# Optimization experiments

Measured on AMD Instinct MI355X. Metric: run time of the kernel, lower is better.

Reference implementation:

```python
import jax, jax.numpy as jnp
import numpy as np

NEG_SLOPE = 0.01
LN_EPS = 1e-5


def leaky_relu(x):
    return jax.nn.leaky_relu(x, NEG_SLOPE)


def layer_norm(x, w, b):
    mu = jnp.mean(x, axis=-1, keepdims=True)
    var = jnp.var(x, axis=-1, keepdims=True)
    return (x - mu) * jax.lax.rsqrt(var + LN_EPS) * w + b


def setup_inputs() -> dict:
    key = jax.random.key(0)
    B, N, IN_DIM, OUT_DIM = 16, 1024, 512, 512
    ks = jax.random.split(key, 12)
    s_in = 1.0 / np.sqrt(IN_DIM)
    s_n = 1.0 / np.sqrt(N)
    return {
        "node_feats": jax.random.normal(ks[0], (B, N, IN_DIM), jnp.float32),
        "adj_matrix": jax.random.uniform(ks[1], (B, N, N), jnp.float32),
        "linear_w": jax.random.uniform(ks[2], (OUT_DIM, IN_DIM), jnp.float32, -s_in, s_in),
        "linear_b": jax.random.uniform(ks[3], (OUT_DIM,), jnp.float32, -s_in, s_in),
        "q_w": jax.random.uniform(ks[4], (N, N), jnp.float32, -s_n, s_n),
        "q_b": jax.random.uniform(ks[5], (N,), jnp.float32, -s_n, s_n),
        "k_w": jax.random.uniform(ks[6], (N, N), jnp.float32, -s_n, s_n),
        "k_b": jax.random.uniform(ks[7], (N,), jnp.float32, -s_n, s_n),
        "v_w": jax.random.uniform(ks[8], (N, N), jnp.float32, -s_n, s_n),
        "v_b": jax.random.uniform(ks[9], (N,), jnp.float32, -s_n, s_n),
        "norm1_w": jnp.ones((N,), jnp.float32),
        "norm1_b": jnp.zeros((N,), jnp.float32),
        "norm2_w": jnp.ones((OUT_DIM,), jnp.float32),
        "norm2_b": jnp.zeros((OUT_DIM,), jnp.float32),
        "edge_weight": jnp.ones((N, N), jnp.float32),
    }


def reference(node_feats, adj_matrix, linear_w, linear_b, q_w, q_b, k_w, k_b,
              v_w, v_b, norm1_w, norm1_b, norm2_w, norm2_b, edge_weight):
    N = edge_weight.shape[0]
    channel_scale = N ** (-0.5)

    # weighted adjacency + symmetric degree normalization (D^-1/2 A D^-1/2)
    W_A = adj_matrix * jax.nn.sigmoid(edge_weight)          # [B,N,N]
    d_inv_sqrt = jnp.power(jnp.sum(W_A, axis=-1), -0.5)     # [B,N]
    d_inv_sqrt = jnp.where(jnp.isinf(d_inv_sqrt), 0.0, d_inv_sqrt)
    W_A = d_inv_sqrt[:, :, None] * W_A * d_inv_sqrt[:, None, :]

    # node projection + channel-wise self-attention
    X = leaky_relu(jnp.einsum('bni,oi->bno', node_feats, linear_w) + linear_b)  # [B,N,O]
    Tx = jnp.swapaxes(X, -1, -2)                             # [B,O,N]
    Tx = layer_norm(Tx, norm1_w, norm1_b)
    q = jnp.einsum('bxh,gh->bxg', Tx, q_w) + q_b
    k = jnp.einsum('bxh,gh->bxg', Tx, k_w) + k_b
    v = leaky_relu(jnp.einsum('bxh,gh->bxg', Tx, v_w) + v_b)
    att = jax.nn.softmax(jnp.einsum('bxh,byh->bxy', q, k) * channel_scale, axis=-1)
    Tx = Tx + jnp.einsum('bxy,byh->bxh', att, v)

    # graph propagation + final norm
    X = jnp.swapaxes(Tx, -1, -2)                             # [B,N,O]
    X = jnp.einsum('bnm,bmo->bno', W_A, X)
    return layer_norm(X, norm2_w, norm2_b)
```

## Files before the change

kernel.cpp:

```cpp
#include <hip/hip_runtime.h>


typedef __bf16 bf16x8 __attribute__((ext_vector_type(8)));
typedef float  f32x4  __attribute__((ext_vector_type(4)));

#define DEV __device__ __forceinline__

DEV float bf2f(unsigned short u) {
  union { unsigned i; float f; } x; x.i = ((unsigned)u) << 16; return x.f;
}
DEV unsigned short f2bf(float f) {
  unsigned u = __float_as_uint(f);
  u += 0x7fffu + ((u >> 16) & 1u);
  return (unsigned short)(u >> 16);
}
DEV float sigmoidf_(float x) { return 1.0f / (1.0f + __expf(-x)); }

DEV float wave_sum(float v) {
#pragma unroll
  for (int o = 32; o > 0; o >>= 1) v += __shfl_xor(v, o, 64);
  return v;
}
DEV float wave_max(float v) {
#pragma unroll
  for (int o = 32; o > 0; o >>= 1) v = fmaxf(v, __shfl_xor(v, o, 64));
  return v;
}

DEV void gload16(const unsigned short* g, unsigned short* l) {
  __builtin_amdgcn_global_load_lds(
      (const __attribute__((address_space(1))) unsigned int*)g,
      (__attribute__((address_space(3))) unsigned int*)l, 16, 0, 0);
}

#define BAR()        asm volatile("s_barrier" ::: "memory")
#define WAIT_VM(n)   asm volatile("s_waitcnt vmcnt(" #n ")" ::: "memory")
#define SB0()        __builtin_amdgcn_sched_barrier(0)

__global__ __launch_bounds__(256) void cast_kernel(const float* __restrict__ in,
                                                   unsigned short* __restrict__ out,
                                                   int n4) {
  int g = blockIdx.x * 256 + threadIdx.x;
  if (g >= n4) return;
  float4 v = *(const float4*)(in + (size_t)g * 4);
  ushort4 o;
  o.x = f2bf(v.x); o.y = f2bf(v.y); o.z = f2bf(v.z); o.w = f2bf(v.w);
  *(ushort4*)(out + (size_t)g * 4) = o;
}

__global__ __launch_bounds__(256) void sigrow_kernel(const float* __restrict__ adj,
                                                     const float* __restrict__ edge,
                                                     float* __restrict__ dis) {
  __shared__ float sh[4];
  size_t row = blockIdx.x;
  int n = (int)(row & 1023);
  const float* ar = adj + row * 1024;
  const float* er = edge + (size_t)n * 1024;
  int c = threadIdx.x * 4;
  float4 a4 = *(const float4*)(ar + c);
  float4 e4 = *(const float4*)(er + c);
  float s = a4.x * sigmoidf_(e4.x) + a4.y * sigmoidf_(e4.y) +
            a4.z * sigmoidf_(e4.z) + a4.w * sigmoidf_(e4.w);
  s = wave_sum(s);
  if ((threadIdx.x & 63) == 0) sh[threadIdx.x >> 6] = s;
  __syncthreads();
  if (threadIdx.x == 0) {
    float t = sh[0] + sh[1] + sh[2] + sh[3];
    dis[row] = t > 0.0f ? rsqrtf(t) : 0.0f;
  }
}

__global__ __launch_bounds__(256) void wa_kernel(const float* __restrict__ adj,
                                                 const float* __restrict__ edge,
                                                 const float* __restrict__ dis,
                                                 unsigned short* __restrict__ wa) {
  size_t g = (size_t)blockIdx.x * 256 + threadIdx.x;
  int m = (int)(g & 255) * 4;
  size_t rest = g >> 8;
  int n = (int)(rest & 1023);
  int b = (int)(rest >> 10);
  float4 a4 = *(const float4*)(adj + rest * 1024 + m);
  float4 e4 = *(const float4*)(edge + (size_t)n * 1024 + m);
  float dn = dis[rest];
  float4 dm = *(const float4*)(dis + (size_t)b * 1024 + m);
  ushort4 o;
  o.x = f2bf(dn * a4.x * sigmoidf_(e4.x) * dm.x);
  o.y = f2bf(dn * a4.y * sigmoidf_(e4.y) * dm.y);
  o.z = f2bf(dn * a4.z * sigmoidf_(e4.z) * dm.z);
  o.w = f2bf(dn * a4.w * sigmoidf_(e4.w) * dm.w);
  *(ushort4*)(wa + g * 4) = o;
}

template <int VPT, bool OUTF32>
__global__ __launch_bounds__(256) void ln_kernel(const unsigned short* __restrict__ in,
                                                 const float* __restrict__ gw,
                                                 const float* __restrict__ gb,
                                                 void* __restrict__ out, int D) {
  __shared__ float sh[8];
  size_t row = blockIdx.x;
  const unsigned short* x = in + row * (size_t)D;
  int base = threadIdx.x * VPT;
  float v[VPT];
  if (VPT == 4) {
    ushort4 u = *(const ushort4*)(x + base);
    v[0] = bf2f(u.x); v[1] = bf2f(u.y); v[2] = bf2f(u.z); v[3] = bf2f(u.w);
  } else {
    ushort2 u = *(const ushort2*)(x + base);
    v[0] = bf2f(u.x); v[1] = bf2f(u.y);
  }
  float s = 0.f, sq = 0.f;
#pragma unroll
  for (int i = 0; i < VPT; i++) { s += v[i]; sq += v[i] * v[i]; }
  s = wave_sum(s); sq = wave_sum(sq);
  if ((threadIdx.x & 63) == 0) { sh[threadIdx.x >> 6] = s; sh[4 + (threadIdx.x >> 6)] = sq; }
  __syncthreads();
  s = sh[0] + sh[1] + sh[2] + sh[3];
  sq = sh[4] + sh[5] + sh[6] + sh[7];
  float mean = s / D;
  float var = sq / D - mean * mean;
  float rs = rsqrtf(fmaxf(var, 0.0f) + 1e-5f);
#pragma unroll
  for (int i = 0; i < VPT; i++) {
    float y = (v[i] - mean) * rs * gw[base + i] + gb[base + i];
    if (OUTF32) ((float*)out)[row * D + base + i] = y;
    else        ((unsigned short*)out)[row * D + base + i] = f2bf(y);
  }
}

__global__ __launch_bounds__(256) void softmax_kernel(const float* __restrict__ in,
                                                      const float* __restrict__ in2,
                                                      unsigned short* __restrict__ out) {
  __shared__ float sh[4];
  size_t row = blockIdx.x;
  const float* x = in + row * 512;
  const float* x2 = in2 + row * 512;
  float2 u = *(const float2*)(x + threadIdx.x * 2);
  float2 u2 = *(const float2*)(x2 + threadIdx.x * 2);
  float a = (u.x + u2.x) * 0.03125f, b = (u.y + u2.y) * 0.03125f;
  float m = wave_max(fmaxf(a, b));
  int wid = threadIdx.x >> 6;
  if ((threadIdx.x & 63) == 0) sh[wid] = m;
  __syncthreads();
  m = fmaxf(fmaxf(sh[0], sh[1]), fmaxf(sh[2], sh[3]));
  __syncthreads();
  float e0 = __expf(a - m), e1 = __expf(b - m);
  float s = wave_sum(e0 + e1);
  if ((threadIdx.x & 63) == 0) sh[wid] = s;
  __syncthreads();
  s = sh[0] + sh[1] + sh[2] + sh[3];
  float inv = 1.0f / s;
  ushort2 o; o.x = f2bf(e0 * inv); o.y = f2bf(e1 * inv);
  *(ushort2*)(out + row * 512 + threadIdx.x * 2) = o;
}

#define MFMA16(d, s0, s1) d = __builtin_amdgcn_mfma_f32_16x16x32_bf16(s0, s1, d, 0, 0, 0)

#define STGA(bi, h, kt) do { \
  gload16(gA + (size_t)((h) * 128) * Kr + (size_t)(kt) * 64, As + (bi) * 16384 + (h) * 8192 + ldst); \
  gload16(gA + (size_t)((h) * 128 + 64) * Kr + (size_t)(kt) * 64, As + (bi) * 16384 + (h) * 8192 + 4096 + ldst); \
} while (0)
#define STGB(bi, h, kt) do { \
  gload16(gB + (size_t)((h) * 128) * Kr + (size_t)(kt) * 64, Bs + (bi) * BSZ + (h) * 8192 + ldst); \
  gload16(gB + (size_t)((h) * 128 + 64) * Kr + (size_t)(kt) * 64, Bs + (bi) * BSZ + (h) * 8192 + 4096 + ldst); \
} while (0)

#define LDA(bi, mh) do { \
  _Pragma("unroll") for (int mf = 0; mf < 4; mf++) { \
    a[mf][0] = *(const bf16x8*)&As[(bi) * 16384 + arow + ((mh) * 4 + mf) * 1024 + xs0]; \
    a[mf][1] = *(const bf16x8*)&As[(bi) * 16384 + arow + ((mh) * 4 + mf) * 1024 + xs1]; \
  } } while (0)
#define LDB(bi, nh) do { \
  if constexpr (BNT == 256) { \
    _Pragma("unroll") for (int nf = 0; nf < 2; nf++) { \
      bb[(nh) * 2 + nf][0] = *(const bf16x8*)&Bs[(bi) * BSZ + brow + ((nh) * 2 + nf) * 1024 + xs0]; \
      bb[(nh) * 2 + nf][1] = *(const bf16x8*)&Bs[(bi) * BSZ + brow + ((nh) * 2 + nf) * 1024 + xs1]; \
    } \
  } else { \
    _Pragma("unroll") for (int nf = 0; nf < 2; nf++) { \
      bb[nf][0] = *(const bf16x8*)&Bs[(bi) * BSZ + brow + nf * 1024 + xs0]; \
      bb[nf][1] = *(const bf16x8*)&Bs[(bi) * BSZ + brow + nf * 1024 + xs1]; \
    } \
  } } while (0)

#define MMQB(mh, nh) do { \
  if constexpr (BNT == 256) { \
    _Pragma("unroll") for (int mf = 0; mf < 4; mf++) \
    _Pragma("unroll") for (int nf = 0; nf < 2; nf++) { \
      MFMA16(acc[(mh) * 4 + mf][(nh) * 2 + nf], a[mf][0], bb[(nh) * 2 + nf][0]); \
      MFMA16(acc[(mh) * 4 + mf][(nh) * 2 + nf], a[mf][1], bb[(nh) * 2 + nf][1]); \
    } \
  } else { \
    _Pragma("unroll") for (int mf = 0; mf < 4; mf++) { \
      MFMA16(acc[(mh) * 4 + mf][(nh)], a[mf][0], bb[(nh)][0]); \
      MFMA16(acc[(mh) * 4 + mf][(nh)], a[mf][1], bb[(nh)][1]); \
    } \
  } } while (0)

#define MMQ2(mh) do { \
  __builtin_amdgcn_s_setprio(1); \
  MMQB(mh, 0); MMQB(mh, 1); \
  __builtin_amdgcn_s_setprio(0); } while (0)

#define TILE2(P, kt, SA, SB, EW) do { \
  EW; BAR(); \
  LDA(P, 0); LDB(P, 0); \
  if constexpr (BNT == 256) { LDB(P, 1); } \
  if (SA) { STGA((P) ^ 1, 0, (kt) + 1); STGA((P) ^ 1, 1, (kt) + 1); } \
  BAR(); SB0(); MMQ2(0); SB0(); BAR(); \
  LDA(P, 1); \
  if (SB) { STGB(P, 0, (kt) + 2); if constexpr (BNT == 256) { STGB(P, 1, (kt) + 2); } } \
  BAR(); SB0(); MMQ2(1); SB0(); \
} while (0)

template <int BNT, int BIAS , bool LEAKY, bool RESID,
          bool OUTF32, bool SPLIT, bool SPLITK>
__global__ __launch_bounds__(512, 2) void gemm256(
    const unsigned short* __restrict__ A, size_t sA,
    const unsigned short* __restrict__ Bt, size_t sB,
    const float* __restrict__ bias, const float* __restrict__ bias2,
    const unsigned short* __restrict__ resid,
    void* __restrict__ out, void* __restrict__ out2,
    int M, int NcS, int K, int Kst, int lgx, int lgy, int xh) {
  constexpr int NFR = (BNT == 256) ? 4 : 2;
  constexpr int BSZ = BNT * 64;
  __shared__ unsigned short As[2 * 16384];
  __shared__ unsigned short Bs[2 * BSZ];
  const int qc = gridDim.x >> 3;
  const int dd = blockIdx.x;
  const int lb = (dd & 7) * qc + (dd >> 3);
  const int x = lb & ((1 << lgx) - 1);
  const int y = (lb >> lgx) & ((1 << lgy) - 1);
  const int b = (lb >> (lgx + lgy)) & 15;
  const int sk = SPLITK ? (lb >> (lgx + lgy + 4)) : 0;

  const int tid = threadIdx.x;
  const int wid = tid >> 6, lane = tid & 63;
  const int wr = wid >> 2, wc = wid & 3;
  const int l15 = lane & 15, l4 = lane >> 4;
  const int tM = y * 256, tN = x * BNT;
  const size_t Kr = (size_t)Kst;

  const int srow = wid * 8 + (lane >> 3);
  const int scol = ((lane & 7) ^ ((lane >> 3) & 7)) * 8;
  const int koff = sk * K;
  const unsigned short* gA = A + sA * b + (size_t)(tM + srow) * Kr + scol + koff;
  const unsigned short* gB = Bt + sB * b + (size_t)(tN + srow) * Kr + scol + koff;
  const int ldst = wid * 512;

  const int xs0 = ((0 * 4 + l4) ^ (lane & 7)) * 8;
  const int xs1 = ((1 * 4 + l4) ^ (lane & 7)) * 8;
  const int arow = (wr * 128 + l15) * 64;
  const int brow = (wc * (BNT / 4) + l15) * 64;

  f32x4 acc[8][NFR] = {};
  bf16x8 a[4][2], bb[NFR][2];

  const int nt = K >> 6;
  STGB(0, 0, 0);
  if constexpr (BNT == 256) { STGB(0, 1, 0); }
  STGA(0, 0, 0); STGA(0, 1, 0);
  STGB(1, 0, 1);
  if constexpr (BNT == 256) { STGB(1, 1, 1); }

  if constexpr (BNT == 256) {
    for (int kt = 0; kt < nt - 2; kt += 2) {
      TILE2(0, kt, true, true, WAIT_VM(4));
      TILE2(1, kt + 1, true, true, WAIT_VM(4));
    }
    TILE2(0, nt - 2, true, false, WAIT_VM(4));
    TILE2(1, nt - 1, false, false, WAIT_VM(0));
  } else {
    for (int kt = 0; kt < nt - 2; kt += 2) {
      TILE2(0, kt, true, true, WAIT_VM(2));
      TILE2(1, kt + 1, true, true, WAIT_VM(2));
    }
    TILE2(0, nt - 2, true, false, WAIT_VM(2));
    TILE2(1, nt - 1, false, false, WAIT_VM(0));
  }

  const float* bia = bias;
  void* o = out;
  if (SPLIT && x >= xh) { bia = bias2; o = out2; }
  if (SPLITK && sk) o = out2;
  const size_t ob = (size_t)M * NcS * b;
#pragma unroll
  for (int mf = 0; mf < 8; mf++)
#pragma unroll
    for (int nf = 0; nf < NFR; nf++) {
      const int cg = tN + wc * (BNT / 4) + nf * 16 + l15;
      const int rbase = tM + wr * 128 + mf * 16 + l4 * 4;
#pragma unroll
      for (int r = 0; r < 4; r++) {
        const int rg = rbase + r;
        float v = acc[mf][nf][r];
        if (BIAS == 1) v += bia[rg];
        if (BIAS == 2) v += bia[cg];
        if (LEAKY) v = v > 0.0f ? v : 0.01f * v;
        const size_t idx = ob + (size_t)rg * NcS + cg;
        if (RESID) v += bf2f(resid[idx]);
        if (OUTF32) ((float*)o)[idx] = v;
        else        ((unsigned short*)o)[idx] = f2bf(v);
      }
    }
}

extern "C" void kernel_launch(void* const* d_in, const int* in_sizes, int n_in,
                              void* d_out, int out_size, void* d_ws, size_t ws_size,
                              hipStream_t stream) {
  const float* node_feats = (const float*)d_in[0];
  const float* adj        = (const float*)d_in[1];
  const float* linear_w   = (const float*)d_in[2];
  const float* linear_b   = (const float*)d_in[3];
  const float* q_w        = (const float*)d_in[4];
  const float* q_b        = (const float*)d_in[5];
  const float* k_w        = (const float*)d_in[6];
  const float* k_b        = (const float*)d_in[7];
  const float* v_w        = (const float*)d_in[8];
  const float* v_b        = (const float*)d_in[9];
  const float* n1w        = (const float*)d_in[10];
  const float* n1b        = (const float*)d_in[11];
  const float* n2w        = (const float*)d_in[12];
  const float* n2b        = (const float*)d_in[13];
  const float* edge       = (const float*)d_in[14];
  float* out = (float*)d_out;

  const int B = 16, N = 1024, C = 512;
  const size_t MiB = 1u << 20;
  char* w = (char*)d_ws;
  unsigned short* nf_bf   = (unsigned short*)(w);
  unsigned short* Xt_bf   = (unsigned short*)(w + 16 * MiB);
  float*          att_raw = (float*)(w);
  float*          att_raw2= (float*)(w + 16 * MiB);
  unsigned short* WA_bf   = (unsigned short*)(w);
  unsigned short* Txln    = (unsigned short*)(w + 32 * MiB);
  unsigned short* q_bf    = (unsigned short*)(w + 48 * MiB);
  unsigned short* X3_bf   = (unsigned short*)(w + 48 * MiB);
  unsigned short* k_bf    = (unsigned short*)(w + 64 * MiB);
  unsigned short* att_bf  = (unsigned short*)(w + 64 * MiB);
  unsigned short* vt_bf   = (unsigned short*)(w + 80 * MiB);
  unsigned short* Tx2_bf  = (unsigned short*)(w + 96 * MiB);
  unsigned short* lw_bf   = (unsigned short*)(w + 112 * MiB);
  unsigned short* qw_bf   = (unsigned short*)(w + 113 * MiB);
  unsigned short* kw_bf   = (unsigned short*)(w + 115 * MiB);
  unsigned short* vw_bf   = (unsigned short*)(w + 117 * MiB);
  float*          dis     = (float*)(w + 119 * MiB);

  cast_kernel<<<(B * N * C / 4 + 255) / 256, 256, 0, stream>>>(node_feats, nf_bf, B * N * C / 4);
  cast_kernel<<<(C * C / 4 + 255) / 256, 256, 0, stream>>>(linear_w, lw_bf, C * C / 4);
  cast_kernel<<<(N * N / 4 + 255) / 256, 256, 0, stream>>>(q_w, qw_bf, N * N / 4);
  cast_kernel<<<(N * N / 4 + 255) / 256, 256, 0, stream>>>(k_w, kw_bf, N * N / 4);
  cast_kernel<<<(N * N / 4 + 255) / 256, 256, 0, stream>>>(v_w, vw_bf, N * N / 4);

  sigrow_kernel<<<B * N, 256, 0, stream>>>(adj, edge, dis);

  gemm256<128, 1, true, false, false, false, false><<<256, 512, 0, stream>>>(
      lw_bf, 0, nf_bf, (size_t)N * C, linear_b, nullptr, nullptr,
      Xt_bf, nullptr, C, N, C, C, 3, 1, 999);

  ln_kernel<4, false><<<B * C, 256, 0, stream>>>(Xt_bf, n1w, n1b, Txln, N);

  gemm256<256, 2, false, false, false, true, false><<<256, 512, 0, stream>>>(
      Txln, (size_t)C * N, qw_bf, 0, q_b, k_b - 1024, nullptr,
      q_bf, (void*)(k_bf - 1024), C, N, N, N, 3, 1, 4);

  gemm256<128, 1, true, false, false, false, false><<<256, 512, 0, stream>>>(
      vw_bf, 0, Txln, (size_t)C * N, v_b, nullptr, nullptr,
      vt_bf, nullptr, N, C, N, N, 2, 2, 999);

  gemm256<128, 0, false, false, true, false, true><<<256, 512, 0, stream>>>(
      q_bf, (size_t)C * N, k_bf, (size_t)C * N, nullptr, nullptr, nullptr,
      att_raw, att_raw2, C, C, 512, N, 2, 1, 999);

  softmax_kernel<<<B * C, 256, 0, stream>>>(att_raw, att_raw2, att_bf);

  wa_kernel<<<B * N * N / 4 / 256, 256, 0, stream>>>(adj, edge, dis, WA_bf);

  gemm256<128, 0, false, true, false, false, false><<<256, 512, 0, stream>>>(
      att_bf, (size_t)C * C, vt_bf, (size_t)N * C, nullptr, nullptr, Txln,
      Tx2_bf, nullptr, C, N, C, C, 3, 1, 999);

  gemm256<128, 0, false, false, false, false, false><<<256, 512, 0, stream>>>(
      WA_bf, (size_t)N * N, Tx2_bf, (size_t)C * N, nullptr, nullptr, nullptr,
      X3_bf, nullptr, N, C, N, N, 2, 2, 999);

  ln_kernel<2, true><<<B * N, 256, 0, stream>>>(X3_bf, n2w, n2b, out, C);
}
```

Baseline: 218.6 us.

## Simplify GEMM main loop to single-barrier double-buffered K pipeline

Replaces the hand-tuned two-phase TILE2 schedule with a simpler TILE1 loop. The old loop had a staggered A/B prefetch, several barriers, sched_barriers and setprio around the MFMA blocks. Each K tile now waits for all outstanding global loads, takes one barrier, issues the next tile's A and B global-to-LDS loads, then runs the MFMAs. This cuts barrier count and scheduling constraints, and snakes the MFMA order for register reuse. In exchange it gives up prefetch depth, since vmcnt(0) each iteration exposes load latency, and it drops the priority and scheduling hints.

```diff
diff --git a/kernel.cpp b/kernel.cpp
--- a/kernel.cpp
+++ b/kernel.cpp
@@ -33,9 +33,8 @@
       (__attribute__((address_space(3))) unsigned int*)l, 16, 0, 0);
 }
 
-#define BAR()        asm volatile("s_barrier" ::: "memory")
+#define BARD()       asm volatile("s_waitcnt lgkmcnt(0)\n\ts_barrier" ::: "memory")
 #define WAIT_VM(n)   asm volatile("s_waitcnt vmcnt(" #n ")" ::: "memory")
-#define SB0()        __builtin_amdgcn_sched_barrier(0)
 
 __global__ __launch_bounds__(256) void cast_kernel(const float* __restrict__ in,
                                                    unsigned short* __restrict__ out,
@@ -196,20 +195,19 @@
     } \
   } } while (0)
 
-#define MMQ2(mh) do { \
-  __builtin_amdgcn_s_setprio(1); \
-  MMQB(mh, 0); MMQB(mh, 1); \
-  __builtin_amdgcn_s_setprio(0); } while (0)
-
-#define TILE2(P, kt, SA, SB, EW) do { \
-  EW; BAR(); \
+#define TILE1(P, kt, SG) do { \
+  WAIT_VM(0); \
+  BARD(); \
+  if (SG) { \
+    STGA((P) ^ 1, 0, (kt) + 1); STGA((P) ^ 1, 1, (kt) + 1); \
+    STGB((P) ^ 1, 0, (kt) + 1); \
+    if constexpr (BNT == 256) { STGB((P) ^ 1, 1, (kt) + 1); } \
+  } \
   LDA(P, 0); LDB(P, 0); \
   if constexpr (BNT == 256) { LDB(P, 1); } \
-  if (SA) { STGA((P) ^ 1, 0, (kt) + 1); STGA((P) ^ 1, 1, (kt) + 1); } \
-  BAR(); SB0(); MMQ2(0); SB0(); BAR(); \
+  MMQB(0, 0); MMQB(0, 1); \
   LDA(P, 1); \
-  if (SB) { STGB(P, 0, (kt) + 2); if constexpr (BNT == 256) { STGB(P, 1, (kt) + 2); } } \
-  BAR(); SB0(); MMQ2(1); SB0(); \
+  MMQB(1, 1); MMQB(1, 0); \
 } while (0)
 
 template <int BNT, int BIAS , bool LEAKY, bool RESID,
@@ -256,27 +254,12 @@
   bf16x8 a[4][2], bb[NFR][2];
 
   const int nt = K >> 6;
+  STGA(0, 0, 0); STGA(0, 1, 0);
   STGB(0, 0, 0);
   if constexpr (BNT == 256) { STGB(0, 1, 0); }
-  STGA(0, 0, 0); STGA(0, 1, 0);
-  STGB(1, 0, 1);
-  if constexpr (BNT == 256) { STGB(1, 1, 1); }
-
-  if constexpr (BNT == 256) {
-    for (int kt = 0; kt < nt - 2; kt += 2) {
-      TILE2(0, kt, true, true, WAIT_VM(4));
-      TILE2(1, kt + 1, true, true, WAIT_VM(4));
-    }
-    TILE2(0, nt - 2, true, false, WAIT_VM(4));
-    TILE2(1, nt - 1, false, false, WAIT_VM(0));
-  } else {
-    for (int kt = 0; kt < nt - 2; kt += 2) {
-      TILE2(0, kt, true, true, WAIT_VM(2));
-      TILE2(1, kt + 1, true, true, WAIT_VM(2));
-    }
-    TILE2(0, nt - 2, true, false, WAIT_VM(2));
-    TILE2(1, nt - 1, false, false, WAIT_VM(0));
-  }
+
+  for (int kt = 0; kt < nt; ++kt)
+    TILE1(kt & 1, kt, kt < nt - 1);
 
   const float* bia = bias;
   void* o = out;
```

Measured after the change: 225.6 us. +3.2%, slower.
